# Performance work log

Measured on AMD Instinct MI355X. Metric: run time of the kernel, lower is better.

## Reference

```python
import jax, jax.numpy as jnp
import numpy as np

N_NODES = 100000
N_EDGES = 1600000
K = 48

def setup_inputs() -> dict:
    key = jax.random.key(0)
    ks = jax.random.split(key, 6)
    x = jax.random.normal(ks[0], (N_NODES, K), dtype=jnp.float32)
    pos_edge_index = jax.random.randint(ks[1], (2, N_EDGES), 0, N_NODES, dtype=jnp.int64)
    neg_edge_index = jax.random.randint(ks[2], (2, N_EDGES), 0, N_NODES, dtype=jnp.int64)
    # nn.Linear-style init (uniform +-1/sqrt(fan_in))
    lim1 = 1.0 / np.sqrt(3 * K)
    W1 = jax.random.uniform(ks[3], (3 * K, 16), minval=-lim1, maxval=lim1, dtype=jnp.float32)
    b1 = jnp.zeros((16,), dtype=jnp.float32)
    lim2 = 1.0 / np.sqrt(16)
    W2 = jax.random.uniform(ks[4], (16, K), minval=-lim2, maxval=lim2, dtype=jnp.float32)
    b2 = jnp.zeros((K,), dtype=jnp.float32)
    return {"x": x, "pos_edge_index": pos_edge_index, "neg_edge_index": neg_edge_index,
            "W1": W1, "b1": b1, "W2": W2, "b2": b2}

def _scatter_add_mp(x, edge_index):
    # PyG MessagePassing(aggr='add'), message = x_j:
    # gather source-node features and scatter-add into target nodes.
    src, dst = edge_index[0], edge_index[1]
    msgs = x[src]  # [E, k]
    return jax.ops.segment_sum(msgs, dst, num_segments=x.shape[0])  # [N, k]

def reference(x, pos_edge_index, neg_edge_index, W1, b1, W2, b2):
    x_pos = _scatter_add_mp(x, pos_edge_index)
    x_neg = _scatter_add_mp(x, neg_edge_index)
    out_cat = jnp.concatenate([x, x_pos, x_neg], axis=1)  # [N, 3k]
    h = jnp.tanh(out_cat @ W1 + b1)                        # [N, 16]
    C = h @ W2 + b2                                        # [N, k]
    return jax.nn.softmax(C, axis=1)
```

## Files before the change

kernel.cpp:

```cpp
#include <hip/hip_runtime.h>
#include <hip/hip_fp16.h>
#include <math.h>

#define NN 100000
#define NE 1600000
#define KF 48
#define NEDGE_ALL (2 * NE)

#define BKT_NODES 128
#define NBKT_PER  782
#define NBKT      1564
#define PACK_EPB  4096
#define NPB       782
#define OT2       1566
#define CAP2      2432
#define KSTG      10

typedef _Float16 half2v __attribute__((ext_vector_type(2)));
typedef _Float16 half4v __attribute__((ext_vector_type(4)));

#if defined(__has_builtin)
#if __has_builtin(__builtin_amdgcn_fdot2)
#define HAVE_FDOT2 1
#endif
#endif

__device__ __forceinline__ void acc_pair(float& ax, float& ay, half2v v)
{
#ifdef HAVE_FDOT2
    ax = __builtin_amdgcn_fdot2(v, (half2v){(_Float16)1.f, (_Float16)0.f}, ax, false);
    ay = __builtin_amdgcn_fdot2(v, (half2v){(_Float16)0.f, (_Float16)1.f}, ay, false);
#else
    ax += (float)v.x;
    ay += (float)v.y;
#endif
}

__global__ __launch_bounds__(512) void pack_kernel(
    const float* __restrict__ x,
    const int* __restrict__ ei_pos,
    const int* __restrict__ ei_neg,
    unsigned short* __restrict__ offT,
    unsigned* __restrict__ plist,
    __half* __restrict__ xh)
{
    {
        const float2* __restrict__ x2 = (const float2*)x;
        half2v* __restrict__ xhw = (half2v*)xh;
        const int n2 = (NN + 2) * (KF / 2);
        for (int i = blockIdx.x * 512 + threadIdx.x; i < n2; i += NPB * 512) {
            float2 v = (i < NN * (KF / 2)) ? x2[i] : make_float2(0.f, 0.f);
            xhw[i] = (half2v){(_Float16)v.x, (_Float16)v.y};
        }
    }

    __shared__ int cnt[NBKT];
    __shared__ int ps[391];
    __shared__ unsigned stage[PACK_EPB];

    const int t = threadIdx.x;
    for (int i = t; i < NBKT; i += 512) cnt[i] = 0;
    __syncthreads();

    unsigned pk[8];
    int bk[8];
    const int blockBase = blockIdx.x * PACK_EPB;
#pragma unroll
    for (int j = 0; j < 8; ++j) {
        int e = blockBase + j * 512 + t;
        bk[j] = -1;
        if (e < NEDGE_ALL) {
            int list = e >= NE;
            int ee = list ? e - NE : e;
            const int* ei = list ? ei_neg : ei_pos;
            int src = ei[ee];
            int dst = ei[NE + ee];
            int b = list * NBKT_PER + (dst >> 7);
            bk[j] = b;
            pk[j] = ((unsigned)(dst & 127) << 17) | (unsigned)src;
            atomicAdd(&cnt[b], 1);
        }
    }
    __syncthreads();

    int s0 = 0, s1 = 0, s2 = 0, s3 = 0;
    if (t < 391) {
        s0 = cnt[4 * t]; s1 = cnt[4 * t + 1]; s2 = cnt[4 * t + 2]; s3 = cnt[4 * t + 3];
        ps[t] = s0 + s1 + s2 + s3;
    }
    __syncthreads();
    for (int d = 1; d < 391; d <<= 1) {
        int v = (t < 391 && t >= d) ? ps[t - d] : 0;
        __syncthreads();
        if (t < 391) ps[t] += v;
        __syncthreads();
    }
    unsigned short* myrow = offT + (long)blockIdx.x * OT2;
    if (t < 391) {
        int base = t ? ps[t - 1] : 0;
        int o0 = base, o1 = o0 + s0, o2 = o1 + s1, o3 = o2 + s2;
        myrow[4 * t]     = (unsigned short)o0;
        myrow[4 * t + 1] = (unsigned short)o1;
        myrow[4 * t + 2] = (unsigned short)o2;
        myrow[4 * t + 3] = (unsigned short)o3;
        cnt[4 * t] = o0; cnt[4 * t + 1] = o1; cnt[4 * t + 2] = o2; cnt[4 * t + 3] = o3;
    }
    if (t == 390) myrow[NBKT] = (unsigned short)ps[390];
    __syncthreads();

#pragma unroll
    for (int j = 0; j < 8; ++j) {
        if (bk[j] >= 0) {
            int slot = atomicAdd(&cnt[bk[j]], 1);
            stage[slot] = pk[j];
        }
    }
    __syncthreads();

    {
        const uint4* __restrict__ st4 = (const uint4*)stage;
        uint4* __restrict__ out4 = (uint4*)(plist + (long)blockIdx.x * PACK_EPB);
#pragma unroll
        for (int j = 0; j < 2; ++j)
            out4[j * 512 + t] = st4[j * 512 + t];
    }
}

__global__ __launch_bounds__(256) void gather_kernel(
    const __half* __restrict__ xh,
    const unsigned* __restrict__ plist,
    const unsigned short* __restrict__ offT,
    float* __restrict__ xpos,
    float* __restrict__ xneg)
{
    __shared__ unsigned srt[CAP2];
    __shared__ int rb[NPB + 2];
    __shared__ unsigned short rsL[NPB];
    __shared__ int tmp[196];
    __shared__ int nh[BKT_NODES];
    __shared__ int starts[BKT_NODES];
    __shared__ int ends[BKT_NODES];
    __shared__ int cur2[BKT_NODES];

    const int b = blockIdx.x;
    const int t = threadIdx.x;

    for (int r = t; r < NPB; r += 256) {
        int s = offT[(long)r * OT2 + b];
        int e = offT[(long)r * OT2 + b + 1];
        rsL[r] = (unsigned short)s;
        srt[r] = (unsigned)(e - s);
    }
    if (t < BKT_NODES) nh[t] = 0;
    __syncthreads();

    int s0 = 0, s1 = 0, s2 = 0, s3 = 0;
    if (t < 196) {
        int i0 = 4 * t;
        s0 = (i0     < NPB) ? (int)srt[i0]     : 0;
        s1 = (i0 + 1 < NPB) ? (int)srt[i0 + 1] : 0;
        s2 = (i0 + 2 < NPB) ? (int)srt[i0 + 2] : 0;
        s3 = (i0 + 3 < NPB) ? (int)srt[i0 + 3] : 0;
        tmp[t] = s0 + s1 + s2 + s3;
    }
    __syncthreads();
    for (int d = 1; d < 196; d <<= 1) {
        int v = (t < 196 && t >= d) ? tmp[t - d] : 0;
        __syncthreads();
        if (t < 196) tmp[t] += v;
        __syncthreads();
    }
    if (t < 196) {
        int base = t ? tmp[t - 1] : 0;
        int i0 = 4 * t;
        if (i0     <= NPB) rb[i0]     = base;
        if (i0 + 1 <= NPB) rb[i0 + 1] = base + s0;
        if (i0 + 2 <= NPB) rb[i0 + 2] = base + s0 + s1;
        if (i0 + 3 <= NPB) rb[i0 + 3] = base + s0 + s1 + s2;
    }
    __syncthreads();
    int cb = rb[NPB];
    if (cb > CAP2) cb = CAP2;

    unsigned held[KSTG];
#pragma unroll
    for (int k = 0; k < KSTG; ++k) {
        int i = t + k * 256;
        held[k] = 0;
        if (i < cb) {
            int lo = 0, hi = NPB - 1;
#pragma unroll
            for (int it = 0; it < 10; ++it) {
                int mid = (lo + hi + 1) >> 1;
                bool ge = (rb[mid] <= i);
                lo = ge ? mid : lo;
                hi = ge ? hi : mid - 1;
            }
            unsigned p = plist[(long)lo * PACK_EPB + rsL[lo] + (i - rb[lo])];
            held[k] = p;
            atomicAdd(&nh[p >> 17], 1);
        }
    }
    __syncthreads();

    for (int d = 1; d < BKT_NODES; d <<= 1) {
        int v = 0;
        if (t < BKT_NODES && t >= d) v = nh[t - d];
        __syncthreads();
        if (t < BKT_NODES) nh[t] += v;
        __syncthreads();
    }
    if (t < BKT_NODES) {
        int e_ = min(nh[t], CAP2);
        int s_ = t ? min(nh[t - 1], CAP2) : 0;
        starts[t] = s_;
        ends[t] = e_;
        cur2[t] = s_;
    }
    __syncthreads();

#pragma unroll
    for (int k = 0; k < KSTG; ++k) {
        int i = t + k * 256;
        if (i < cb) {
            unsigned p = held[k];
            int slot = atomicAdd(&cur2[p >> 17], 1);
            if (slot < CAP2) srt[slot] = p;
        }
    }
    __syncthreads();

    const int wave = t >> 6, lane = t & 63;
    const int g = lane >> 4;
    const int sub = lane & 15;
    const int subc = (sub < 12) ? sub : 11;
    const int list = b >= NBKT_PER;
    const int nb = list ? b - NBKT_PER : b;
    float* o = list ? xneg : xpos;
    const half4v* __restrict__ xh4 = (const half4v*)xh;

    for (int n = wave; n < BKT_NODES; n += 4) {
        int gn = nb * BKT_NODES + n;
        if (gn >= NN) continue;
        int s = starts[n], e = ends[n];
        float a0 = 0.f, a1 = 0.f, a2 = 0.f, a3 = 0.f;
        for (int j = s; j < e; j += 16) {
            int i0 = j + g, i1 = j + 4 + g, i2 = j + 8 + g, i3 = j + 12 + g;
            int q0 = (i0 < e) ? (int)(srt[i0 < CAP2 ? i0 : 0] & 0x1FFFFu) : NN;
            int q1 = (i1 < e) ? (int)(srt[i1 < CAP2 ? i1 : 0] & 0x1FFFFu) : NN;
            int q2 = (i2 < e) ? (int)(srt[i2 < CAP2 ? i2 : 0] & 0x1FFFFu) : NN;
            int q3 = (i3 < e) ? (int)(srt[i3 < CAP2 ? i3 : 0] & 0x1FFFFu) : NN;
            half4v v0 = xh4[q0 * 12 + subc];
            half4v v1 = xh4[q1 * 12 + subc];
            half4v v2 = xh4[q2 * 12 + subc];
            half4v v3 = xh4[q3 * 12 + subc];
            acc_pair(a0, a1, (half2v){v0.x, v0.y});
            acc_pair(a2, a3, (half2v){v0.z, v0.w});
            acc_pair(a0, a1, (half2v){v1.x, v1.y});
            acc_pair(a2, a3, (half2v){v1.z, v1.w});
            acc_pair(a0, a1, (half2v){v2.x, v2.y});
            acc_pair(a2, a3, (half2v){v2.z, v2.w});
            acc_pair(a0, a1, (half2v){v3.x, v3.y});
            acc_pair(a2, a3, (half2v){v3.z, v3.w});
        }
        a0 += __shfl_xor(a0, 16); a0 += __shfl_xor(a0, 32);
        a1 += __shfl_xor(a1, 16); a1 += __shfl_xor(a1, 32);
        a2 += __shfl_xor(a2, 16); a2 += __shfl_xor(a2, 32);
        a3 += __shfl_xor(a3, 16); a3 += __shfl_xor(a3, 32);
        if (g == 0 && sub < 12) {
            float4* o4 = (float4*)o;
            o4[(long)gn * 12 + sub] = make_float4(a0, a1, a2, a3);
        }
    }
}

__global__ __launch_bounds__(256) void scatter2_kernel(
    const float* __restrict__ x,
    const int* __restrict__ ei_pos,
    const int* __restrict__ ei_neg,
    float* acc_pos,
    float* acc_neg)
{
    const int list = blockIdx.y;
    const int* ei = list ? ei_neg : ei_pos;
    float* acc = list ? acc_neg : acc_pos;

    long t = (long)blockIdx.x * blockDim.x + threadIdx.x;
    const long total = (long)NE * 12;
    if (t >= total) return;

    int e = (int)(t / 12);
    int r = (int)(t - (long)e * 12);
    int k4 = r * 4;

    int src = ei[e];
    int dst = ei[NE + e];

    const float4 v = *(const float4*)(x + (long)src * KF + k4);
    float* p = acc + (long)dst * KF + k4;

    unsafeAtomicAdd(p + 0, v.x);
    unsafeAtomicAdd(p + 1, v.y);
    unsafeAtomicAdd(p + 2, v.z);
    unsafeAtomicAdd(p + 3, v.w);
}

__global__ __launch_bounds__(256) void mlp_softmax_kernel(
    const float* __restrict__ x,
    const float* xpos,
    const float* __restrict__ xneg,
    const float* __restrict__ W1,
    const float* __restrict__ b1,
    const float* __restrict__ W2,
    const float* __restrict__ b2,
    float* out)
{
    __shared__ float sW1[144 * 16];
    __shared__ float sW2[16 * 48];
    __shared__ float sb1[16];
    __shared__ float sb2[48];

    for (int i = threadIdx.x; i < 144 * 16; i += blockDim.x) sW1[i] = W1[i];
    for (int i = threadIdx.x; i < 16 * 48;  i += blockDim.x) sW2[i] = W2[i];
    if (threadIdx.x < 16) sb1[threadIdx.x] = b1[threadIdx.x];
    if (threadIdx.x < 48) sb2[threadIdx.x] = b2[threadIdx.x];
    __syncthreads();

    const int n = blockIdx.x * blockDim.x + threadIdx.x;
    if (n >= NN) return;

    float h[16];
#pragma unroll
    for (int j = 0; j < 16; ++j) h[j] = sb1[j];

    const float* srcs[3];
    srcs[0] = x    + (long)n * KF;
    srcs[1] = xpos + (long)n * KF;
    srcs[2] = xneg + (long)n * KF;

    for (int s = 0; s < 3; ++s) {
        const float* px = srcs[s];
        for (int i = 0; i < KF; ++i) {
            const float v = px[i];
            const float* w = &sW1[(s * KF + i) * 16];
#pragma unroll
            for (int j = 0; j < 16; ++j) h[j] += v * w[j];
        }
    }
#pragma unroll
    for (int j = 0; j < 16; ++j) h[j] = tanhf(h[j]);

    float C[KF];
#pragma unroll
    for (int k = 0; k < KF; ++k) C[k] = sb2[k];
    for (int j = 0; j < 16; ++j) {
        const float hv = h[j];
        const float* w = &sW2[j * KF];
#pragma unroll
        for (int k = 0; k < KF; ++k) C[k] += hv * w[k];
    }

    float m = C[0];
#pragma unroll
    for (int k = 1; k < KF; ++k) m = fmaxf(m, C[k]);
    float ssum = 0.f;
#pragma unroll
    for (int k = 0; k < KF; ++k) { C[k] = expf(C[k] - m); ssum += C[k]; }
    const float inv = 1.0f / ssum;

    float* po = out + (long)n * KF;
#pragma unroll
    for (int k = 0; k < KF; ++k) po[k] = C[k] * inv;
}

extern "C" void kernel_launch(void* const* d_in, const int* in_sizes, int n_in,
                              void* d_out, int out_size, void* d_ws, size_t ws_size,
                              hipStream_t stream)
{
    const float* x      = (const float*)d_in[0];
    const int*   ei_pos = (const int*)  d_in[1];
    const int*   ei_neg = (const int*)  d_in[2];
    const float* W1     = (const float*)d_in[3];
    const float* b1     = (const float*)d_in[4];
    const float* W2     = (const float*)d_in[5];
    const float* b2     = (const float*)d_in[6];

    float* out  = (float*)d_out;
    float* xpos = (float*)d_out;

    const size_t acc_bytes   = (size_t)NN * KF * sizeof(float);
    const size_t plist_bytes = (size_t)NPB * PACK_EPB * sizeof(unsigned);
    const size_t offT_bytes  = (size_t)NPB * OT2 * sizeof(unsigned short);
    const size_t xh_bytes    = (size_t)(NN + 2) * KF * sizeof(__half);

    size_t off = 0;
    char* ws = (char*)d_ws;
    float*          xneg  = (float*)(ws + off);          off += acc_bytes;
    unsigned*       plist = (unsigned*)(ws + off);       off += plist_bytes;
    unsigned short* offT  = (unsigned short*)(ws + off); off += offT_bytes;
    __half*         xh    = (__half*)(ws + off);         off += xh_bytes;
    const size_t needed = off;

    if (ws_size >= needed) {
        pack_kernel<<<NPB, 512, 0, stream>>>(x, ei_pos, ei_neg, offT, plist, xh);
        gather_kernel<<<NBKT, 256, 0, stream>>>(xh, plist, offT, xpos, xneg);
    } else {
        hipMemsetAsync(xpos, 0, acc_bytes, stream);
        hipMemsetAsync(xneg, 0, acc_bytes, stream);
        const long total = (long)NE * 12;
        dim3 grid((unsigned)((total + 255) / 256), 2, 1);
        scatter2_kernel<<<grid, 256, 0, stream>>>(x, ei_pos, ei_neg, xpos, xneg);
    }

    mlp_softmax_kernel<<<(NN + 255) / 256, 256, 0, stream>>>(x, xpos, xneg, W1, b1, W2, b2, out);
}
```

Before: 235.2 us.

## Double pack block size and transpose offset table for coalesced gather reads

```diff
diff --git a/kernel.cpp b/kernel.cpp
--- a/kernel.cpp
+++ b/kernel.cpp
@@ -10,9 +10,10 @@
 #define BKT_NODES 128
 #define NBKT_PER  782
 #define NBKT      1564
-#define PACK_EPB  4096
-#define NPB       782
-#define OT2       1566
+#define PACK_EPB  8192
+#define NPB       391
+#define OTR       1565
+#define OTT       392
 #define CAP2      2432
 #define KSTG      10
 
@@ -36,7 +37,7 @@
 #endif
 }
 
-__global__ __launch_bounds__(512) void pack_kernel(
+__global__ __launch_bounds__(1024) void pack_kernel(
     const float* __restrict__ x,
     const int* __restrict__ ei_pos,
     const int* __restrict__ ei_neg,
@@ -48,7 +49,7 @@
         const float2* __restrict__ x2 = (const float2*)x;
         half2v* __restrict__ xhw = (half2v*)xh;
         const int n2 = (NN + 2) * (KF / 2);
-        for (int i = blockIdx.x * 512 + threadIdx.x; i < n2; i += NPB * 512) {
+        for (int i = blockIdx.x * 1024 + threadIdx.x; i < n2; i += NPB * 1024) {
             float2 v = (i < NN * (KF / 2)) ? x2[i] : make_float2(0.f, 0.f);
             xhw[i] = (half2v){(_Float16)v.x, (_Float16)v.y};
         }
@@ -59,7 +60,7 @@
     __shared__ unsigned stage[PACK_EPB];
 
     const int t = threadIdx.x;
-    for (int i = t; i < NBKT; i += 512) cnt[i] = 0;
+    for (int i = t; i < NBKT; i += 1024) cnt[i] = 0;
     __syncthreads();
 
     unsigned pk[8];
@@ -67,7 +68,7 @@
     const int blockBase = blockIdx.x * PACK_EPB;
 #pragma unroll
     for (int j = 0; j < 8; ++j) {
-        int e = blockBase + j * 512 + t;
+        int e = blockBase + j * 1024 + t;
         bk[j] = -1;
         if (e < NEDGE_ALL) {
             int list = e >= NE;
@@ -95,7 +96,7 @@
         if (t < 391) ps[t] += v;
         __syncthreads();
     }
-    unsigned short* myrow = offT + (long)blockIdx.x * OT2;
+    unsigned short* myrow = offT + (long)blockIdx.x * OTR;
     if (t < 391) {
         int base = t ? ps[t - 1] : 0;
         int o0 = base, o1 = o0 + s0, o2 = o1 + s1, o3 = o2 + s2;
@@ -116,27 +117,54 @@
         }
     }
     __syncthreads();
-
     {
         const uint4* __restrict__ st4 = (const uint4*)stage;
         uint4* __restrict__ out4 = (uint4*)(plist + (long)blockIdx.x * PACK_EPB);
 #pragma unroll
         for (int j = 0; j < 2; ++j)
-            out4[j * 512 + t] = st4[j * 512 + t];
+            out4[j * 1024 + t] = st4[j * 1024 + t];
+    }
+}
+
+__global__ __launch_bounds__(256) void transpose_kernel(
+    const unsigned short* __restrict__ offT,
+    unsigned short* __restrict__ offTt)
+{
+    __shared__ unsigned short tile[32 * 65];
+    const int rt = blockIdx.x;
+    const int bt = blockIdx.y;
+    const int t = threadIdx.x;
+
+#pragma unroll
+    for (int k = 0; k < 8; ++k) {
+        int q = t + k * 256;
+        int rl_ = q >> 6, bl_ = q & 63;
+        int gr = rt * 32 + rl_, gb = bt * 64 + bl_;
+        if (gr < NPB && gb < NBKT + 1)
+            tile[rl_ * 65 + bl_] = offT[(long)gr * OTR + gb];
+    }
+    __syncthreads();
+#pragma unroll
+    for (int k = 0; k < 8; ++k) {
+        int q = t + k * 256;
+        int bl_ = q >> 5, rl_ = q & 31;
+        int gb = bt * 64 + bl_, gr = rt * 32 + rl_;
+        if (gr < NPB && gb < NBKT + 1)
+            offTt[(long)gb * OTT + gr] = tile[rl_ * 65 + bl_];
     }
 }
 
 __global__ __launch_bounds__(256) void gather_kernel(
     const __half* __restrict__ xh,
     const unsigned* __restrict__ plist,
-    const unsigned short* __restrict__ offT,
+    const unsigned short* __restrict__ offTt,
     float* __restrict__ xpos,
     float* __restrict__ xneg)
 {
     __shared__ unsigned srt[CAP2];
-    __shared__ int rb[NPB + 2];
+    __shared__ int rb[NPB + 1];
     __shared__ unsigned short rsL[NPB];
-    __shared__ int tmp[196];
+    __shared__ int tmp[98];
     __shared__ int nh[BKT_NODES];
     __shared__ int starts[BKT_NODES];
     __shared__ int ends[BKT_NODES];
@@ -146,8 +174,8 @@
     const int t = threadIdx.x;
 
     for (int r = t; r < NPB; r += 256) {
-        int s = offT[(long)r * OT2 + b];
-        int e = offT[(long)r * OT2 + b + 1];
+        int s = offTt[(long)b * OTT + r];
+        int e = offTt[(long)(b + 1) * OTT + r];
         rsL[r] = (unsigned short)s;
         srt[r] = (unsigned)(e - s);
     }
@@ -155,7 +183,7 @@
     __syncthreads();
 
     int s0 = 0, s1 = 0, s2 = 0, s3 = 0;
-    if (t < 196) {
+    if (t < 98) {
         int i0 = 4 * t;
         s0 = (i0     < NPB) ? (int)srt[i0]     : 0;
         s1 = (i0 + 1 < NPB) ? (int)srt[i0 + 1] : 0;
@@ -164,13 +192,13 @@
         tmp[t] = s0 + s1 + s2 + s3;
     }
     __syncthreads();
-    for (int d = 1; d < 196; d <<= 1) {
-        int v = (t < 196 && t >= d) ? tmp[t - d] : 0;
-        __syncthreads();
-        if (t < 196) tmp[t] += v;
-        __syncthreads();
-    }
-    if (t < 196) {
+    for (int d = 1; d < 98; d <<= 1) {
+        int v = (t < 98 && t >= d) ? tmp[t - d] : 0;
+        __syncthreads();
+        if (t < 98) tmp[t] += v;
+        __syncthreads();
+    }
+    if (t < 98) {
         int base = t ? tmp[t - 1] : 0;
         int i0 = 4 * t;
         if (i0     <= NPB) rb[i0]     = base;
@@ -190,7 +218,7 @@
         if (i < cb) {
             int lo = 0, hi = NPB - 1;
 #pragma unroll
-            for (int it = 0; it < 10; ++it) {
+            for (int it = 0; it < 9; ++it) {
                 int mid = (lo + hi + 1) >> 1;
                 bool ge = (rb[mid] <= i);
                 lo = ge ? mid : lo;
@@ -390,7 +418,8 @@
 
     const size_t acc_bytes   = (size_t)NN * KF * sizeof(float);
     const size_t plist_bytes = (size_t)NPB * PACK_EPB * sizeof(unsigned);
-    const size_t offT_bytes  = (size_t)NPB * OT2 * sizeof(unsigned short);
+    const size_t offT_bytes  = (size_t)NPB * OTR * sizeof(unsigned short);
+    const size_t offTt_bytes = (size_t)(NBKT + 1) * OTT * sizeof(unsigned short);
     const size_t xh_bytes    = (size_t)(NN + 2) * KF * sizeof(__half);
 
     size_t off = 0;
@@ -398,12 +427,14 @@
     float*          xneg  = (float*)(ws + off);          off += acc_bytes;
     unsigned*       plist = (unsigned*)(ws + off);       off += plist_bytes;
     unsigned short* offT  = (unsigned short*)(ws + off); off += offT_bytes;
+    unsigned short* offTt = (unsigned short*)(ws + off); off += offTt_bytes;
     __half*         xh    = (__half*)(ws + off);         off += xh_bytes;
     const size_t needed = off;
 
     if (ws_size >= needed) {
-        pack_kernel<<<NPB, 512, 0, stream>>>(x, ei_pos, ei_neg, offT, plist, xh);
-        gather_kernel<<<NBKT, 256, 0, stream>>>(xh, plist, offT, xpos, xneg);
+        pack_kernel<<<NPB, 1024, 0, stream>>>(x, ei_pos, ei_neg, offT, plist, xh);
+        transpose_kernel<<<dim3(13, 25), 256, 0, stream>>>(offT, offTt);
+        gather_kernel<<<NBKT, 256, 0, stream>>>(xh, plist, offTt, xpos, xneg);
     } else {
         hipMemsetAsync(xpos, 0, acc_bytes, stream);
         hipMemsetAsync(xneg, 0, acc_bytes, stream);
```

Measured after the change: 246.4 us. 1.05x slower.
